# Performance work log

Hardware: AMD Instinct MI355X
Metric: run time of the kernel (lower is better)

The kernel has to match this reference:

```python
import jax, jax.numpy as jnp
import numpy as np

N = 100000
D = 128


def segment_mean(x, idx, n):
    s = jax.ops.segment_sum(x, idx, num_segments=n)
    c = jax.ops.segment_sum(jnp.ones((idx.shape[0],), x.dtype), idx, num_segments=n)
    return s / jnp.maximum(c, 1.0)[:, None]


def setup_inputs() -> dict:
    key = jax.random.key(0)
    ks = jax.random.split(key, 10)
    scale = 1.0 / np.sqrt(D)
    return {
        "embedding": jax.random.normal(ks[0], (N, D), dtype=jnp.float32),
        "W_down": jax.random.normal(ks[1], (D, D), dtype=jnp.float32) * scale,
        "b_down": jnp.zeros((D,), dtype=jnp.float32),
        "W_gcn": jax.random.normal(ks[2], (D, D), dtype=jnp.float32) * scale,
        "b_gcn": jnp.zeros((D,), dtype=jnp.float32),
        "W_up": jax.random.normal(ks[3], (D, D), dtype=jnp.float32) * scale,
        "b_up": jnp.zeros((D,), dtype=jnp.float32),
        "down2up_path": jax.random.randint(ks[4], (2, 100000), 0, N),
        "same_level_edge_index": jax.random.randint(ks[5], (2, 600000), 0, N),
        "up2down_edge_index": jax.random.randint(ks[6], (2, 100000), 0, N),
    }


def _forward(embedding, W_down, b_down, W_gcn, b_gcn, W_up, b_up,
             down2up_path, same_level_edge_index, up2down_edge_index):
    # ---- Down2Up: aggregate children into parents (mean), transform, residual add ----
    src, dst = down2up_path[0], down2up_path[1]
    agg = segment_mean(embedding[src], dst, N)                     # [N, D]
    x = jax.nn.relu(embedding + agg @ W_down + b_down)

    # ---- Same-level GCNConv with self-loops and symmetric normalization ----
    s, d = same_level_edge_index[0], same_level_edge_index[1]
    h = x @ W_gcn                                                  # [N, D]
    deg = jax.ops.segment_sum(jnp.ones((s.shape[0],), h.dtype), d, num_segments=N) + 1.0
    dinv = jax.lax.rsqrt(deg)                                      # deg^{-1/2}
    norm = dinv[s] * dinv[d]                                       # [E]
    x = jax.ops.segment_sum(norm[:, None] * h[s], d, num_segments=N)
    x = x + h * (1.0 / deg)[:, None] + b_gcn                       # self-loop term

    # ---- Up2Down: propagate parents back down to children (mean), transform, residual ----
    src2, dst2 = up2down_edge_index[0], up2down_edge_index[1]
    agg2 = segment_mean(x[src2], dst2, N)
    return jax.nn.relu(x + agg2 @ W_up + b_up)


def reference(embedding, W_down, b_down, W_gcn, b_gcn, W_up, b_up,
              down2up_path, same_level_edge_index, up2down_edge_index):
    return _forward(embedding, W_down, b_down, W_gcn, b_gcn, W_up, b_up,
                    down2up_path, same_level_edge_index, up2down_edge_index)
```

## Files before the change

kernel.cpp:

```cpp
#include <hip/hip_runtime.h>
#include <cstdint>
#include <cstddef>

#define NNODES 100000
#define DIM 128
#define TLD 144

#define NB3   (3 * NNODES)
#define BSH   9
#define NBUCK ((NB3 + 511) >> 9)
#define EPB   2048

typedef unsigned short u16;
typedef uint32_t u32;
typedef __attribute__((ext_vector_type(8))) short v8s;
typedef __attribute__((ext_vector_type(4))) float v4f;

__device__ __forceinline__ float bf2f(u32 u) {
  union { u32 i; float f; } x; x.i = u << 16; return x.f;
}
__device__ __forceinline__ u16 f2bf(float f) {
  union { float f; u32 i; } x; x.f = f;
  u32 r = x.i + 0x7fffu + ((x.i >> 16) & 1u);
  return (u16)(r >> 16);
}
__device__ __forceinline__ u32 packsplit(float f) {
  u16 h = f2bf(f);
  float r = f - bf2f(h);
  u16 l = f2bf(r);
  return (u32)h | ((u32)l << 16);
}


__global__ __launch_bounds__(256) void bin_count(const int* __restrict__ d2u,
    const int* __restrict__ sle, const int* __restrict__ u2d,
    int E1, int E2, int E3, int* __restrict__ bcnt) {
  __shared__ int lc[NBUCK];
  const int tid = threadIdx.x;
  for (int i = tid; i < NBUCK; i += 256) lc[i] = 0;
  __syncthreads();
  const int Etot = E1 + E2 + E3;
  const int base = blockIdx.x * EPB;
#pragma unroll
  for (int k = 0; k < EPB; k += 256) {
    int e = base + k + tid;
    if (e < Etot) {
      int idx;
      if (e < E1)            idx = d2u[E1 + e];
      else if (e < E1 + E2)  idx = NNODES + sle[E2 + (e - E1)];
      else                   idx = 2 * NNODES + u2d[E3 + (e - E1 - E2)];
      atomicAdd(&lc[idx >> BSH], 1);
    }
  }
  __syncthreads();
  for (int i = tid; i < NBUCK; i += 256)
    if (lc[i]) atomicAdd(&bcnt[i], lc[i]);
}

__global__ void bin_scan(const int* __restrict__ bcnt, int* __restrict__ brs,
                         int* __restrict__ bfill) {
  __shared__ int tmp[1024];
  const int tid = threadIdx.x;
  for (int i = tid; i < 1024; i += 256) tmp[i] = (i < NBUCK) ? bcnt[i] : 0;
  __syncthreads();
  for (int off = 1; off < 1024; off <<= 1) {
    int vals[4];
#pragma unroll
    for (int j = 0; j < 4; ++j) { int i = tid + j * 256; vals[j] = (i >= off) ? tmp[i - off] : 0; }
    __syncthreads();
#pragma unroll
    for (int j = 0; j < 4; ++j) { int i = tid + j * 256; tmp[i] += vals[j]; }
    __syncthreads();
  }
  for (int i = tid; i < NBUCK; i += 256) {
    int excl = tmp[i] - bcnt[i];
    brs[i] = excl;
    bfill[i] = excl;
  }
}

__global__ __launch_bounds__(256) void bin_fill(const int* __restrict__ d2u,
    const int* __restrict__ sle, const int* __restrict__ u2d,
    int E1, int E2, int E3, int* __restrict__ bfill, uint2* __restrict__ pairs) {
  __shared__ int lc[NBUCK];
  const int tid = threadIdx.x;
  for (int i = tid; i < NBUCK; i += 256) lc[i] = 0;
  __syncthreads();
  const int Etot = E1 + E2 + E3;
  const int base = blockIdx.x * EPB;
  int vidx[EPB / 256], vsrc[EPB / 256];
#pragma unroll
  for (int k = 0; k < EPB / 256; ++k) {
    int e = base + k * 256 + tid;
    int idx = -1, src = 0;
    if (e < Etot) {
      if (e < E1)            { idx = d2u[E1 + e];                          src = d2u[e]; }
      else if (e < E1 + E2)  { int q = e - E1;      idx = NNODES + sle[E2 + q];      src = sle[q]; }
      else                   { int q = e - E1 - E2; idx = 2 * NNODES + u2d[E3 + q];  src = u2d[q]; }
      atomicAdd(&lc[idx >> BSH], 1);
    }
    vidx[k] = idx; vsrc[k] = src;
  }
  __syncthreads();
  for (int i = tid; i < NBUCK; i += 256) {
    int c = lc[i];
    if (c) lc[i] = atomicAdd(&bfill[i], c);
  }
  __syncthreads();
#pragma unroll
  for (int k = 0; k < EPB / 256; ++k) {
    int idx = vidx[k];
    if (idx >= 0) {
      int pos = atomicAdd(&lc[idx >> BSH], 1);
      pairs[pos] = make_uint2((unsigned)idx, (unsigned)vsrc[k]);
    }
  }
}

__global__ __launch_bounds__(256) void node_count(const uint2* __restrict__ pairs,
    const int* __restrict__ brs, const int* __restrict__ bcnt, int* __restrict__ cnt) {
  __shared__ int c[512];
  const int tid = threadIdx.x;
  const int b = blockIdx.x;
  for (int i = tid; i < 512; i += 256) c[i] = 0;
  __syncthreads();
  const int s = brs[b], m = bcnt[b];
  for (int k = tid; k < m; k += 256) {
    uint2 p = pairs[s + k];
    atomicAdd(&c[p.x & 511], 1);
  }
  __syncthreads();
  const int node0 = b << BSH;
  for (int i = tid; i < 512; i += 256) {
    int g = node0 + i;
    if (g < NB3) cnt[g] = c[i];
  }
}

__global__ __launch_bounds__(256) void scatter_bucket(const uint2* __restrict__ pairs,
    const int* __restrict__ brs, const int* __restrict__ bcnt,
    const int* __restrict__ rs, int* __restrict__ eidx) {
  __shared__ int cur[512];
  const int tid = threadIdx.x;
  const int b = blockIdx.x;
  const int node0 = b << BSH;
  for (int i = tid; i < 512; i += 256) {
    int g = node0 + i;
    cur[i] = (g < NB3) ? rs[g] : 0;
  }
  __syncthreads();
  const int s = brs[b], m = bcnt[b];
  for (int k = tid; k < m; k += 256) {
    uint2 p = pairs[s + k];
    int pos = atomicAdd(&cur[p.x & 511], 1);
    eidx[pos] = (int)p.y;
  }
}


__global__ void scan_blocks(const int* __restrict__ in, int* __restrict__ out,
                            int* __restrict__ bsum, int n) {
  __shared__ int wsum[4];
  const int tid = threadIdx.x;
  const int base = blockIdx.x * 1024 + tid * 4;
  int v0 = 0, v1 = 0, v2 = 0, v3 = 0;
  if (base + 0 < n) v0 = in[base + 0];
  if (base + 1 < n) v1 = in[base + 1];
  if (base + 2 < n) v2 = in[base + 2];
  if (base + 3 < n) v3 = in[base + 3];
  const int tsum = v0 + v1 + v2 + v3;
  const int lane = tid & 63, wid = tid >> 6;
  int x = tsum;
  for (int off = 1; off < 64; off <<= 1) {
    int y = __shfl_up(x, off, 64);
    if (lane >= off) x += y;
  }
  if (lane == 63) wsum[wid] = x;
  __syncthreads();
  int woff = 0;
  for (int w = 0; w < wid; ++w) woff += wsum[w];
  const int excl = woff + x - tsum;
  if (base + 0 < n) out[base + 0] = excl;
  if (base + 1 < n) out[base + 1] = excl + v0;
  if (base + 2 < n) out[base + 2] = excl + v0 + v1;
  if (base + 3 < n) out[base + 3] = excl + v0 + v1 + v2;
  if (tid == 255) bsum[blockIdx.x] = woff + x;
}

__global__ void scan_top(int* __restrict__ bsum, int nb) {
  __shared__ int tmp[1024];
  const int tid = threadIdx.x;
  for (int i = tid; i < 1024; i += 256) tmp[i] = (i < nb) ? bsum[i] : 0;
  __syncthreads();
  for (int off = 1; off < 1024; off <<= 1) {
    int vals[4];
#pragma unroll
    for (int j = 0; j < 4; ++j) { int i = tid + j * 256; vals[j] = (i >= off) ? tmp[i - off] : 0; }
    __syncthreads();
#pragma unroll
    for (int j = 0; j < 4; ++j) { int i = tid + j * 256; tmp[i] += vals[j]; }
    __syncthreads();
  }
  for (int i = tid; i < nb; i += 256) {
    int orig = bsum[i];
    bsum[i] = tmp[i] - orig;
  }
}

__global__ void scan_add(int* __restrict__ out, const int* __restrict__ bsum, int n) {
  const int b = blockIdx.x;
  const int off = bsum[b];
  const int base = b * 1024 + threadIdx.x * 4;
#pragma unroll
  for (int j = 0; j < 4; ++j)
    if (base + j < n) out[base + j] += off;
}

__global__ void make_rnorm(const int* __restrict__ cntB, float* __restrict__ rnorm, int n) {
  int i = blockIdx.x * 256 + threadIdx.x;
  if (i < n) rnorm[i] = rsqrtf((float)cntB[i] + 1.0f);
}

__global__ void make_w_planes(const float* __restrict__ W0, const float* __restrict__ W1,
                              const float* __restrict__ W2,
                              u16* __restrict__ Whi, u16* __restrict__ Wlo) {
  int i = blockIdx.x * 256 + threadIdx.x;
  if (i >= 3 * DIM * DIM) return;
  int j = i & 7, lane = (i >> 3) & 63, ct = (i >> 9) & 7, kk = (i >> 12) & 3, m = i >> 14;
  int lr = lane & 15, quad = lane >> 4;
  int c = ct * 16 + lr;
  int k = kk * 32 + quad * 8 + j;
  const float* W = (m == 0) ? W0 : ((m == 1) ? W1 : W2);
  u32 p = packsplit(W[k * DIM + c]);
  Whi[i] = (u16)(p & 0xffffu);
  Wlo[i] = (u16)(p >> 16);
}


__global__ void gather_gcn(const u16* __restrict__ g,
                           const int* __restrict__ rs, const int* __restrict__ cnt,
                           const int* __restrict__ eidx, const float* __restrict__ rnorm,
                           const float* __restrict__ bias, float* __restrict__ out, int n) {
  int gid = blockIdx.x * 256 + threadIdx.x;
  int i = gid >> 6;
  if (i >= n) return;
  int sub = gid & 63;
  int c = (sub & 31) << 2;
  int start = rs[i], m = cnt[i];
  float4 acc = {0.f, 0.f, 0.f, 0.f};
  if (sub < 32) {
    ushort4 pv = *(const ushort4*)(g + ((size_t)i << 7) + c);
    acc.x = bf2f(pv.x); acc.y = bf2f(pv.y);
    acc.z = bf2f(pv.z); acc.w = bf2f(pv.w);
  }
  int j = sub >> 5;
  for (; j + 2 < m; j += 4) {
    int s0 = eidx[start + j], s1 = eidx[start + j + 2];
    ushort4 p0 = *(const ushort4*)(g + ((size_t)s0 << 7) + c);
    ushort4 p1 = *(const ushort4*)(g + ((size_t)s1 << 7) + c);
    acc.x += bf2f(p0.x) + bf2f(p1.x);
    acc.y += bf2f(p0.y) + bf2f(p1.y);
    acc.z += bf2f(p0.z) + bf2f(p1.z);
    acc.w += bf2f(p0.w) + bf2f(p1.w);
  }
  if (j < m) {
    int s = eidx[start + j];
    ushort4 pv = *(const ushort4*)(g + ((size_t)s << 7) + c);
    acc.x += bf2f(pv.x); acc.y += bf2f(pv.y);
    acc.z += bf2f(pv.z); acc.w += bf2f(pv.w);
  }
  acc.x += __shfl_xor(acc.x, 32);
  acc.y += __shfl_xor(acc.y, 32);
  acc.z += __shfl_xor(acc.z, 32);
  acc.w += __shfl_xor(acc.w, 32);
  if (sub < 32) {
    float ri = rnorm[i];
    float4 bv = *(const float4*)(bias + c);
    float4 o;
    o.x = fmaf(ri, acc.x, bv.x);
    o.y = fmaf(ri, acc.y, bv.y);
    o.z = fmaf(ri, acc.z, bv.z);
    o.w = fmaf(ri, acc.w, bv.w);
    *(float4*)(out + (size_t)i * DIM + c) = o;
  }
}

__global__ __launch_bounds__(512) void fused_ab(
    const float* __restrict__ emb,
    const int* __restrict__ rs, const int* __restrict__ cnt, const int* __restrict__ eidx,
    const u16* __restrict__ Wdh, const u16* __restrict__ Wdl,
    const u16* __restrict__ Wgh, const u16* __restrict__ Wgl,
    const float* __restrict__ bd, const float* __restrict__ rnorm,
    u16* __restrict__ obf, int nrows)
{
  __shared__ u16 S[32768];
  u32* X = (u32*)(S + 16384);
  const int tid = threadIdx.x;
  const int wave = tid >> 6, lane = tid & 63;
  const int lr = lane & 15, quad = lane >> 4;
  const int rowbase = blockIdx.x * 128 + wave * 16;

  int arow = rowbase + lr;
  if (arow >= nrows) arow = nrows - 1;
  const int start = rs[arow], m = cnt[arow];
  float4 fa[4], fb[4];
#pragma unroll
  for (int kk = 0; kk < 4; ++kk) {
    fa[kk] = (float4){0.f, 0.f, 0.f, 0.f};
    fb[kk] = (float4){0.f, 0.f, 0.f, 0.f};
  }
  for (int j = 0; j < m; ++j) {
    int s = eidx[start + j];
    const float* rp = emb + (size_t)s * DIM + quad * 8;
#pragma unroll
    for (int kk = 0; kk < 4; ++kk) {
      float4 v0 = *(const float4*)(rp + kk * 32);
      float4 v1 = *(const float4*)(rp + kk * 32 + 4);
      fa[kk].x += v0.x; fa[kk].y += v0.y; fa[kk].z += v0.z; fa[kk].w += v0.w;
      fb[kk].x += v1.x; fb[kk].y += v1.y; fb[kk].z += v1.z; fb[kk].w += v1.w;
    }
  }
  const float inv = 1.0f / fmaxf((float)m, 1.0f);
  v8s afh[4], afl[4];
#pragma unroll
  for (int kk = 0; kk < 4; ++kk) {
    float vs[8] = {fa[kk].x, fa[kk].y, fa[kk].z, fa[kk].w,
                   fb[kk].x, fb[kk].y, fb[kk].z, fb[kk].w};
#pragma unroll
    for (int j = 0; j < 8; ++j) {
      u32 p = packsplit(vs[j] * inv);
      afh[kk][j] = (short)(p & 0xffffu);
      afl[kk][j] = (short)(p >> 16);
    }
  }

  {
    uint4* S4 = (uint4*)S;
    for (int i = tid; i < 2048; i += 512) {
      S4[i] = ((const uint4*)Wdh)[i];
      S4[2048 + i] = ((const uint4*)Wdl)[i];
    }
  }
  __syncthreads();

  v4f acc[8];
#pragma unroll
  for (int ct = 0; ct < 8; ++ct) acc[ct] = (v4f){0.f, 0.f, 0.f, 0.f};
#pragma unroll
  for (int kk = 0; kk < 4; ++kk) {
#pragma unroll
    for (int ct = 0; ct < 8; ++ct) {
      const int wo = ((kk * 8 + ct) << 9) + (lane << 3);
      v8s bh = *(const v8s*)(S + wo);
      v8s bl = *(const v8s*)(S + 16384 + wo);
      acc[ct] = __builtin_amdgcn_mfma_f32_16x16x32_bf16(afh[kk], bh, acc[ct], 0, 0, 0);
      acc[ct] = __builtin_amdgcn_mfma_f32_16x16x32_bf16(afh[kk], bl, acc[ct], 0, 0, 0);
      acc[ct] = __builtin_amdgcn_mfma_f32_16x16x32_bf16(afl[kk], bh, acc[ct], 0, 0, 0);
    }
  }
  __syncthreads();

  {
    uint4* S4 = (uint4*)S;
    for (int i = tid; i < 2048; i += 512)
      S4[i] = ((const uint4*)Wgh)[i];
  }

#pragma unroll
  for (int cl = 0; cl < 2; ++cl) {
#pragma unroll
    for (int rg = 0; rg < 4; ++rg) {
      int r = rowbase + quad * 4 + rg;
      int rc = (r < nrows) ? r : (nrows - 1);
      const int col = cl * 16 + lr;
      float v = acc[cl][rg] + bd[col] + emb[(size_t)rc * DIM + col];
      v = fmaxf(v, 0.f);
      int slot = ((rg << 1) | cl) * 64 + (quad << 4) + lr;
      slot ^= ((slot >> 6) & 7) << 2;
      X[wave * 512 + slot] = packsplit(v);
    }
  }
  __syncthreads();

  v4f acc2[8];
#pragma unroll
  for (int ct = 0; ct < 8; ++ct) acc2[ct] = (v4f){0.f, 0.f, 0.f, 0.f};
#pragma unroll
  for (int Q = 0; Q < 4; ++Q) {
    v8s agh, agl;
    {
      int s0 = ((lr & 3) * 2 + (quad >> 1)) * 64 + ((lr >> 2) << 4) + ((quad & 1) << 3);
      int s1 = s0 + 4;
      s0 ^= ((s0 >> 6) & 7) << 2;
      s1 ^= ((s1 >> 6) & 7) << 2;
      uint4 q0 = *(const uint4*)(X + wave * 512 + s0);
      uint4 q1 = *(const uint4*)(X + wave * 512 + s1);
      u32 u[8] = {q0.x, q0.y, q0.z, q0.w, q1.x, q1.y, q1.z, q1.w};
#pragma unroll
      for (int j = 0; j < 8; ++j) {
        agh[j] = (short)(u[j] & 0xffffu);
        agl[j] = (short)(u[j] >> 16);
      }
    }
#pragma unroll
    for (int ct = 0; ct < 8; ++ct) {
      const int wo = ((Q * 8 + ct) << 9) + (lane << 3);
      v8s bh = *(const v8s*)(S + wo);
      v8s bl = *(const v8s*)(Wgl + wo);
      acc2[ct] = __builtin_amdgcn_mfma_f32_16x16x32_bf16(agh, bh, acc2[ct], 0, 0, 0);
      acc2[ct] = __builtin_amdgcn_mfma_f32_16x16x32_bf16(agh, bl, acc2[ct], 0, 0, 0);
      acc2[ct] = __builtin_amdgcn_mfma_f32_16x16x32_bf16(agl, bh, acc2[ct], 0, 0, 0);
    }
    if (Q < 3) {
#pragma unroll
      for (int cl = 0; cl < 2; ++cl) {
        int ct = 2 * (Q + 1) + cl;
#pragma unroll
        for (int rg = 0; rg < 4; ++rg) {
          int r = rowbase + quad * 4 + rg;
          int rc = (r < nrows) ? r : (nrows - 1);
          const int col = ct * 16 + lr;
          float v = acc[ct][rg] + bd[col] + emb[(size_t)rc * DIM + col];
          v = fmaxf(v, 0.f);
          int slot = ((rg << 1) | cl) * 64 + (quad << 4) + lr;
          slot ^= ((slot >> 6) & 7) << 2;
          X[wave * 512 + slot] = packsplit(v);
        }
      }
    }
  }

  __syncthreads();

  const int lrow0 = wave * 16 + quad * 4;
#pragma unroll
  for (int rg = 0; rg < 4; ++rg) {
    int lrow = lrow0 + rg;
    int r = blockIdx.x * 128 + lrow;
    float sc = rnorm[(r < nrows) ? r : (nrows - 1)];
#pragma unroll
    for (int ct = 0; ct < 8; ++ct) {
      S[lrow * TLD + ct * 16 + lr] = f2bf(acc2[ct][rg] * sc);
    }
  }
  __syncthreads();
  const int rowstart = blockIdx.x * 128;
  for (int idx = tid; idx < 128 * 16; idx += 512) {
    int lrow = idx >> 4, c8 = (idx & 15) << 3;
    int r = rowstart + lrow;
    if (r < nrows)
      *(uint4*)(obf + ((size_t)r << 7) + c8) = *(const uint4*)&S[lrow * TLD + c8];
  }
}

__global__ __launch_bounds__(512) void gather_gemm_c(
    const float* __restrict__ x,
    const int* __restrict__ rs, const int* __restrict__ cnt, const int* __restrict__ eidx,
    const u16* __restrict__ Wuh, const u16* __restrict__ Wul,
    const float* __restrict__ bias, float* __restrict__ outf, int nrows)
{
  __shared__ u16 W[2 * DIM * DIM];
  const int tid = threadIdx.x;
  const int wave = tid >> 6, lane = tid & 63;
  const int lr = lane & 15, quad = lane >> 4;
  const int rowbase = blockIdx.x * 128 + wave * 16;

  int arow = rowbase + lr;
  if (arow >= nrows) arow = nrows - 1;
  const int start = rs[arow], m = cnt[arow];
  float4 fa[4], fb[4];
#pragma unroll
  for (int kk = 0; kk < 4; ++kk) {
    fa[kk] = (float4){0.f, 0.f, 0.f, 0.f};
    fb[kk] = (float4){0.f, 0.f, 0.f, 0.f};
  }
  for (int j = 0; j < m; ++j) {
    int s = eidx[start + j];
    const float* rp = x + (size_t)s * DIM + quad * 8;
#pragma unroll
    for (int kk = 0; kk < 4; ++kk) {
      float4 v0 = *(const float4*)(rp + kk * 32);
      float4 v1 = *(const float4*)(rp + kk * 32 + 4);
      fa[kk].x += v0.x; fa[kk].y += v0.y; fa[kk].z += v0.z; fa[kk].w += v0.w;
      fb[kk].x += v1.x; fb[kk].y += v1.y; fb[kk].z += v1.z; fb[kk].w += v1.w;
    }
  }
  const float inv = 1.0f / fmaxf((float)m, 1.0f);
  v8s afh[4], afl[4];
#pragma unroll
  for (int kk = 0; kk < 4; ++kk) {
    float vs[8] = {fa[kk].x, fa[kk].y, fa[kk].z, fa[kk].w,
                   fb[kk].x, fb[kk].y, fb[kk].z, fb[kk].w};
#pragma unroll
    for (int j = 0; j < 8; ++j) {
      u32 p = packsplit(vs[j] * inv);
      afh[kk][j] = (short)(p & 0xffffu);
      afl[kk][j] = (short)(p >> 16);
    }
  }

  {
    uint4* W4 = (uint4*)W;
    for (int i = tid; i < 2048; i += 512) {
      W4[i] = ((const uint4*)Wuh)[i];
      W4[2048 + i] = ((const uint4*)Wul)[i];
    }
  }
  __syncthreads();

  v4f acc[8];
#pragma unroll
  for (int ct = 0; ct < 8; ++ct) acc[ct] = (v4f){0.f, 0.f, 0.f, 0.f};
#pragma unroll
  for (int kk = 0; kk < 4; ++kk) {
#pragma unroll
    for (int ct = 0; ct < 8; ++ct) {
      const int wo = ((kk * 8 + ct) << 9) + (lane << 3);
      v8s bh = *(const v8s*)(W + wo);
      v8s bl = *(const v8s*)(W + DIM * DIM + wo);
      acc[ct] = __builtin_amdgcn_mfma_f32_16x16x32_bf16(afh[kk], bh, acc[ct], 0, 0, 0);
      acc[ct] = __builtin_amdgcn_mfma_f32_16x16x32_bf16(afh[kk], bl, acc[ct], 0, 0, 0);
      acc[ct] = __builtin_amdgcn_mfma_f32_16x16x32_bf16(afl[kk], bh, acc[ct], 0, 0, 0);
    }
  }

#pragma unroll
  for (int ct = 0; ct < 8; ++ct) {
    const int col = ct * 16 + lr;
    float bv = bias[col];
#pragma unroll
    for (int rg = 0; rg < 4; ++rg) {
      int r = rowbase + quad * 4 + rg;
      if (r < nrows) {
        size_t off = (size_t)r * DIM + col;
        float v = acc[ct][rg] + bv + x[off];
        outf[off] = fmaxf(v, 0.f);
      }
    }
  }
}


extern "C" void kernel_launch(void* const* d_in, const int* in_sizes, int n_in,
                              void* d_out, int out_size, void* d_ws, size_t ws_size,
                              hipStream_t stream) {
  const float* emb = (const float*)d_in[0];
  const float* Wd  = (const float*)d_in[1];
  const float* bd  = (const float*)d_in[2];
  const float* Wg  = (const float*)d_in[3];
  const float* bg  = (const float*)d_in[4];
  const float* Wu  = (const float*)d_in[5];
  const float* bu  = (const float*)d_in[6];
  const int* d2u = (const int*)d_in[7];
  const int* sle = (const int*)d_in[8];
  const int* u2d = (const int*)d_in[9];
  const int E1 = in_sizes[7] / 2;
  const int E2 = in_sizes[8] / 2;
  const int E3 = in_sizes[9] / 2;
  const int Etot = E1 + E2 + E3;
  const int N  = NNODES;
  const size_t nd = (size_t)N * DIM;

  float* xb = (float*)d_ws;
  u16* Gbf  = (u16*)(xb + nd);
  int* cnt  = (int*)(Gbf + nd);
  int* bbuf = cnt + 3 * N;
  int* rs   = bbuf + 3 * 1024;
  int* eidx = rs + 3 * N;
  float* rnorm = (float*)(eidx + Etot);
  int* bsum = (int*)(rnorm + N);
  u16* Whi = (u16*)(bsum + 1024);
  u16* Wlo = Whi + 3 * DIM * DIM;
  uint2* pairs = (uint2*)(Wlo + 3 * DIM * DIM);
  int* bcnt  = bbuf;
  int* brs   = bbuf + 1024;
  int* bfill = bbuf + 2048;

  const int gemm_blocks = (N + 127) / 128;
  const int nscan = (3 * N + 1023) / 1024;
  const int ngcn = (N * 64 + 255) / 256;
  const int nbin = (Etot + EPB - 1) / EPB;

  (void)hipMemsetAsync(bcnt, 0, 1024 * sizeof(int), stream);
  make_w_planes<<<(3 * DIM * DIM + 255) / 256, 256, 0, stream>>>(Wd, Wg, Wu, Whi, Wlo);
  bin_count<<<nbin, 256, 0, stream>>>(d2u, sle, u2d, E1, E2, E3, bcnt);
  bin_scan<<<1, 256, 0, stream>>>(bcnt, brs, bfill);
  bin_fill<<<nbin, 256, 0, stream>>>(d2u, sle, u2d, E1, E2, E3, bfill, pairs);
  node_count<<<NBUCK, 256, 0, stream>>>(pairs, brs, bcnt, cnt);
  make_rnorm<<<(N + 255) / 256, 256, 0, stream>>>(cnt + N, rnorm, N);
  scan_blocks<<<nscan, 256, 0, stream>>>(cnt, rs, bsum, 3 * N);
  scan_top<<<1, 256, 0, stream>>>(bsum, nscan);
  scan_add<<<nscan, 256, 0, stream>>>(rs, bsum, 3 * N);
  scatter_bucket<<<NBUCK, 256, 0, stream>>>(pairs, brs, bcnt, rs, eidx);

  fused_ab<<<gemm_blocks, 512, 0, stream>>>(emb, rs, cnt, eidx,
                                            Whi, Wlo, Whi + DIM * DIM, Wlo + DIM * DIM,
                                            bd, rnorm, Gbf, N);

  gather_gcn<<<ngcn, 256, 0, stream>>>(Gbf, rs + N, cnt + N, eidx, rnorm, bg, xb, N);

  gather_gemm_c<<<gemm_blocks, 512, 0, stream>>>(xb, rs + 2 * N, cnt + 2 * N, eidx,
                                                 Whi + 2 * DIM * DIM, Wlo + 2 * DIM * DIM,
                                                 bu, (float*)d_out, N);
}
```

Before: 291.3 us.

## Trim launches, prefetch weight planes into registers, swizzle output staging tile

Removes the memset, make_rnorm and scan_top launches. bcnt is now zeroed inside make_w_planes, and scan_add computes each block's offset by summing earlier block sums itself and also writes rnorm. Both fused GEMM kernels load their bf16 weight planes into registers before the gather loop, so those global loads overlap the edge gathers. The output staging tile drops the padded stride for an XOR-swizzled layout to save LDS. The risks are extra register pressure from the prefetch and redundant block-sum reads in scan_add.

```diff
diff --git a/kernel.cpp b/kernel.cpp
--- a/kernel.cpp
+++ b/kernel.cpp
@@ -4,7 +4,6 @@
 
 #define NNODES 100000
 #define DIM 128
-#define TLD 144
 
 #define NB3   (3 * NNODES)
 #define BSH   9
@@ -187,44 +186,36 @@
   if (tid == 255) bsum[blockIdx.x] = woff + x;
 }
 
-__global__ void scan_top(int* __restrict__ bsum, int nb) {
-  __shared__ int tmp[1024];
-  const int tid = threadIdx.x;
-  for (int i = tid; i < 1024; i += 256) tmp[i] = (i < nb) ? bsum[i] : 0;
-  __syncthreads();
-  for (int off = 1; off < 1024; off <<= 1) {
-    int vals[4];
-#pragma unroll
-    for (int j = 0; j < 4; ++j) { int i = tid + j * 256; vals[j] = (i >= off) ? tmp[i - off] : 0; }
-    __syncthreads();
-#pragma unroll
-    for (int j = 0; j < 4; ++j) { int i = tid + j * 256; tmp[i] += vals[j]; }
-    __syncthreads();
-  }
-  for (int i = tid; i < nb; i += 256) {
-    int orig = bsum[i];
-    bsum[i] = tmp[i] - orig;
-  }
-}
-
-__global__ void scan_add(int* __restrict__ out, const int* __restrict__ bsum, int n) {
+__global__ void scan_add(int* __restrict__ rs, const int* __restrict__ bsum,
+                         const int* __restrict__ cnt, float* __restrict__ rnorm, int n) {
+  __shared__ int wsum[4];
   const int b = blockIdx.x;
-  const int off = bsum[b];
-  const int base = b * 1024 + threadIdx.x * 4;
-#pragma unroll
-  for (int j = 0; j < 4; ++j)
-    if (base + j < n) out[base + j] += off;
-}
-
-__global__ void make_rnorm(const int* __restrict__ cntB, float* __restrict__ rnorm, int n) {
-  int i = blockIdx.x * 256 + threadIdx.x;
-  if (i < n) rnorm[i] = rsqrtf((float)cntB[i] + 1.0f);
+  const int tid = threadIdx.x;
+  int s = 0;
+  for (int i = tid; i < b; i += 256) s += bsum[i];
+#pragma unroll
+  for (int o = 32; o > 0; o >>= 1) s += __shfl_down(s, o, 64);
+  if ((tid & 63) == 0) wsum[tid >> 6] = s;
+  __syncthreads();
+  const int off = wsum[0] + wsum[1] + wsum[2] + wsum[3];
+  const int base = b * 1024 + tid * 4;
+#pragma unroll
+  for (int j = 0; j < 4; ++j) {
+    int i = base + j;
+    if (i < n) {
+      rs[i] += off;
+      if (i >= NNODES && i < 2 * NNODES)
+        rnorm[i - NNODES] = rsqrtf((float)cnt[i] + 1.0f);
+    }
+  }
 }
 
 __global__ void make_w_planes(const float* __restrict__ W0, const float* __restrict__ W1,
                               const float* __restrict__ W2,
-                              u16* __restrict__ Whi, u16* __restrict__ Wlo) {
+                              u16* __restrict__ Whi, u16* __restrict__ Wlo,
+                              int* __restrict__ bcnt) {
   int i = blockIdx.x * 256 + threadIdx.x;
+  if (i < 1024) bcnt[i] = 0;
   if (i >= 3 * DIM * DIM) return;
   int j = i & 7, lane = (i >> 3) & 63, ct = (i >> 9) & 7, kk = (i >> 12) & 3, m = i >> 14;
   int lr = lane & 15, quad = lane >> 4;
@@ -303,6 +294,20 @@
   int arow = rowbase + lr;
   if (arow >= nrows) arow = nrows - 1;
   const int start = rs[arow], m = cnt[arow];
+
+  uint4 wd[8], wg[4];
+  {
+    const uint4* H4 = (const uint4*)Wdh;
+    const uint4* L4 = (const uint4*)Wdl;
+    const uint4* G4 = (const uint4*)Wgh;
+#pragma unroll
+    for (int t = 0; t < 4; ++t) {
+      wd[t] = H4[tid + t * 512];
+      wd[4 + t] = L4[tid + t * 512];
+      wg[t] = G4[tid + t * 512];
+    }
+  }
+
   float4 fa[4], fb[4];
 #pragma unroll
   for (int kk = 0; kk < 4; ++kk) {
@@ -336,9 +341,10 @@
 
   {
     uint4* S4 = (uint4*)S;
-    for (int i = tid; i < 2048; i += 512) {
-      S4[i] = ((const uint4*)Wdh)[i];
-      S4[2048 + i] = ((const uint4*)Wdl)[i];
+#pragma unroll
+    for (int t = 0; t < 4; ++t) {
+      S4[tid + t * 512] = wd[t];
+      S4[2048 + tid + t * 512] = wd[4 + t];
     }
   }
   __syncthreads();
@@ -362,8 +368,9 @@
 
   {
     uint4* S4 = (uint4*)S;
-    for (int i = tid; i < 2048; i += 512)
-      S4[i] = ((const uint4*)Wgh)[i];
+#pragma unroll
+    for (int t = 0; t < 4; ++t)
+      S4[tid + t * 512] = wg[t];
   }
 
 #pragma unroll
@@ -438,18 +445,22 @@
     int lrow = lrow0 + rg;
     int r = blockIdx.x * 128 + lrow;
     float sc = rnorm[(r < nrows) ? r : (nrows - 1)];
+    const int swz = (lrow & 7) << 4;
 #pragma unroll
     for (int ct = 0; ct < 8; ++ct) {
-      S[lrow * TLD + ct * 16 + lr] = f2bf(acc2[ct][rg] * sc);
+      const int col = ct * 16 + lr;
+      S[(lrow << 7) + (col ^ swz)] = f2bf(acc2[ct][rg] * sc);
     }
   }
   __syncthreads();
   const int rowstart = blockIdx.x * 128;
-  for (int idx = tid; idx < 128 * 16; idx += 512) {
+  for (int idx = tid; idx < 2048; idx += 512) {
     int lrow = idx >> 4, c8 = (idx & 15) << 3;
     int r = rowstart + lrow;
-    if (r < nrows)
-      *(uint4*)(obf + ((size_t)r << 7) + c8) = *(const uint4*)&S[lrow * TLD + c8];
+    if (r < nrows) {
+      uint4 v = *(const uint4*)&S[(lrow << 7) + (c8 ^ ((lrow & 7) << 4))];
+      *(uint4*)(obf + ((size_t)r << 7) + c8) = v;
+    }
   }
 }
 
@@ -468,6 +479,18 @@
   int arow = rowbase + lr;
   if (arow >= nrows) arow = nrows - 1;
   const int start = rs[arow], m = cnt[arow];
+
+  uint4 wreg[8];
+  {
+    const uint4* H4 = (const uint4*)Wuh;
+    const uint4* L4 = (const uint4*)Wul;
+#pragma unroll
+    for (int t = 0; t < 4; ++t) {
+      wreg[t] = H4[tid + t * 512];
+      wreg[4 + t] = L4[tid + t * 512];
+    }
+  }
+
   float4 fa[4], fb[4];
 #pragma unroll
   for (int kk = 0; kk < 4; ++kk) {
@@ -501,9 +524,10 @@
 
   {
     uint4* W4 = (uint4*)W;
-    for (int i = tid; i < 2048; i += 512) {
-      W4[i] = ((const uint4*)Wuh)[i];
-      W4[2048 + i] = ((const uint4*)Wul)[i];
+#pragma unroll
+    for (int t = 0; t < 4; ++t) {
+      W4[tid + t * 512] = wreg[t];
+      W4[2048 + tid + t * 512] = wreg[4 + t];
     }
   }
   __syncthreads();
@@ -581,16 +605,13 @@
   const int ngcn = (N * 64 + 255) / 256;
   const int nbin = (Etot + EPB - 1) / EPB;
 
-  (void)hipMemsetAsync(bcnt, 0, 1024 * sizeof(int), stream);
-  make_w_planes<<<(3 * DIM * DIM + 255) / 256, 256, 0, stream>>>(Wd, Wg, Wu, Whi, Wlo);
+  make_w_planes<<<(3 * DIM * DIM + 255) / 256, 256, 0, stream>>>(Wd, Wg, Wu, Whi, Wlo, bcnt);
   bin_count<<<nbin, 256, 0, stream>>>(d2u, sle, u2d, E1, E2, E3, bcnt);
   bin_scan<<<1, 256, 0, stream>>>(bcnt, brs, bfill);
   bin_fill<<<nbin, 256, 0, stream>>>(d2u, sle, u2d, E1, E2, E3, bfill, pairs);
   node_count<<<NBUCK, 256, 0, stream>>>(pairs, brs, bcnt, cnt);
-  make_rnorm<<<(N + 255) / 256, 256, 0, stream>>>(cnt + N, rnorm, N);
   scan_blocks<<<nscan, 256, 0, stream>>>(cnt, rs, bsum, 3 * N);
-  scan_top<<<1, 256, 0, stream>>>(bsum, nscan);
-  scan_add<<<nscan, 256, 0, stream>>>(rs, bsum, 3 * N);
+  scan_add<<<nscan, 256, 0, stream>>>(rs, bsum, cnt, rnorm, 3 * N);
   scatter_bucket<<<NBUCK, 256, 0, stream>>>(pairs, brs, bcnt, rs, eidx);
 
   fused_ab<<<gemm_blocks, 512, 0, stream>>>(emb, rs, cnt, eidx,
```

After: 296.4 us. No clear change (+1.7%).
